# Optimization experiments

Hardware: AMD Instinct MI355X
Metric: run time of the kernel (lower is better)

The kernel has to match this reference:

```python
import jax, jax.numpy as jnp
import numpy as np
from jax import lax

ALPHA = 0.85
C1 = 0.01 ** 2
C2 = 0.03 ** 2


def _avg_pool3(x):
    # F.avg_pool2d(x, 3, 1, 1) with count_include_pad=True: zero-pad, divide by 9.
    s = lax.reduce_window(x, jnp.array(0.0, x.dtype), lax.add,
                          (1, 1, 3, 3), (1, 1, 1, 1),
                          [(0, 0), (0, 0), (1, 1), (1, 1)])
    return s / jnp.array(9.0, x.dtype)


def _ssim(x, y):
    mu_x = _avg_pool3(x)
    mu_y = _avg_pool3(y)
    sigma_x = jnp.clip(_avg_pool3(x * x) - mu_x * mu_x, 0.0, None)
    sigma_y = jnp.clip(_avg_pool3(y * y) - mu_y * mu_y, 0.0, None)
    sigma_xy = _avg_pool3(x * y) - mu_x * mu_y
    ssim_n = (2.0 * mu_x * mu_y + C1) * (2.0 * sigma_xy + C2)
    ssim_d = (mu_x * mu_x + mu_y * mu_y + C1) * (sigma_x + sigma_y + C2)
    return jnp.clip((1.0 - ssim_n / ssim_d) / 2.0, 0.0, 1.0)


def _warp_right(right_img, disp):
    # grid_sample(bilinear, border, align_corners=True) where y maps identically
    # to its own row -> a 1D horizontal bilinear gather at x_sample = x - disp.
    B, C, H, W = right_img.shape
    x_base = jnp.arange(W, dtype=disp.dtype).reshape(1, 1, 1, W)
    x_sample = x_base - disp                      # [B,1,H,W]
    xs = jnp.clip(x_sample, 0.0, W - 1.0)         # border padding
    x0 = jnp.floor(xs)
    w = xs - x0                                   # frac weight
    i0 = x0.astype(jnp.int32)
    i1 = jnp.minimum(i0 + 1, W - 1)
    i0b = jnp.broadcast_to(i0, (B, C, H, W))
    i1b = jnp.broadcast_to(i1, (B, C, H, W))
    g0 = jnp.take_along_axis(right_img, i0b, axis=3)
    g1 = jnp.take_along_axis(right_img, i1b, axis=3)
    warped = (1.0 - w) * g0 + w * g1              # w broadcasts over C
    valid = ((x_sample > 0) & (x_sample < W - 1)).astype(disp.dtype)
    return warped, valid


def setup_inputs() -> dict:
    key = jax.random.key(0)
    k1, k2, k3 = jax.random.split(key, 3)
    B, H, W = 8, 720, 1280
    disp = jax.random.normal(k1, (B, 1, H, W), dtype=jnp.float32)
    left_img = jax.random.uniform(k2, (B, 3, H, W), dtype=jnp.float32)
    right_img = jax.random.uniform(k3, (B, 3, H, W), dtype=jnp.float32)
    return {"disp": disp, "left_img": left_img, "right_img": right_img}


def reference(disp, left_img, right_img):
    right_warped, valid = _warp_right(right_img, disp)
    l1_err = jnp.mean(jnp.abs(left_img - right_warped), axis=1, keepdims=True)
    ssim_err = jnp.mean(_ssim(left_img, right_warped), axis=1, keepdims=True)
    photo_err = ALPHA * ssim_err + (1.0 - ALPHA) * l1_err
    n_valid = jnp.maximum(jnp.sum(valid), 1.0)
    return jnp.sum(photo_err * valid) / n_valid
```

## Files before the change

### kernel.cpp

```cpp
#include <hip/hip_runtime.h>


#define P_ALPHA 0.85f
#define P_C1 1e-4f
#define P_C2 9e-4f

constexpr int W_ = 1280, H_ = 720, HW_ = W_ * H_;
constexpr int UCOLS = 62;
constexpr int RPW   = 12;
constexpr int XS    = 21;
constexpr int YS    = H_ / RPW;
constexpr int TASKS = XS * YS * 8;
constexpr int HALF  = TASKS / 2;
constexpr int NB    = HALF / 4;

__global__ __launch_bounds__(256, 5)
void photo_loss_kernel(const float* __restrict__ disp,
                       const float* __restrict__ left,
                       const float* __restrict__ right,
                       float* __restrict__ acc)
{
    __shared__ float redpv[4], redv[4];

    const int tid  = threadIdx.x;
    const int lane = tid & 63;
    const int wv   = tid >> 6;
    const int wgid = blockIdx.x * 4 + wv;
    const float wm1 = (float)(W_ - 1);

    float sum_pv = 0.f, sum_v = 0.f;

    for (int half = 0; half < 2; ++half) {
        const int t   = wgid + half * HALF;
        const int xs  = t % XS;
        const int rem = t / XS;
        const int ys  = rem % YS;
        const int b   = rem / YS;

        const int base = xs * UCOLS;
        const int col  = base + lane - 1;
        const int r0   = ys * RPW;

        const float* __restrict__ dispb = disp + (size_t)b * HW_;
        const float* __restrict__ L0 = left  + (size_t)(b * 3 + 0) * HW_;
        const float* __restrict__ L1 = left  + (size_t)(b * 3 + 1) * HW_;
        const float* __restrict__ L2 = left  + (size_t)(b * 3 + 2) * HW_;
        const float* __restrict__ R0 = right + (size_t)(b * 3 + 0) * HW_;
        const float* __restrict__ R1 = right + (size_t)(b * 3 + 1) * HW_;
        const float* __restrict__ R2 = right + (size_t)(b * 3 + 2) * HW_;

        const int   colC = min(max(col, 0), W_ - 1);
        const float colv = (col >= 0 && col < W_) ? 1.f : 0.f;
        const float ocm  = (lane >= 1 && lane <= UCOLS && col < W_) ? 1.f : 0.f;

        float rsx[3][3], rsy[3][3], rsxx[3][3], rsyy[3][3], rsxy[3][3];
        float l1r[3], vr[3];

        auto emit = [&](int cs) {
            const float inv9 = 1.f / 9.f;
            float ssim_sum = 0.f;
            #pragma unroll
            for (int c = 0; c < 3; ++c) {
                float mu_x = (rsx[c][0]  + rsx[c][1]  + rsx[c][2])  * inv9;
                float mu_y = (rsy[c][0]  + rsy[c][1]  + rsy[c][2])  * inv9;
                float exx  = (rsxx[c][0] + rsxx[c][1] + rsxx[c][2]) * inv9;
                float eyy  = (rsyy[c][0] + rsyy[c][1] + rsyy[c][2]) * inv9;
                float exy  = (rsxy[c][0] + rsxy[c][1] + rsxy[c][2]) * inv9;
                float sig_x  = fmaxf(exx - mu_x * mu_x, 0.f);
                float sig_y  = fmaxf(eyy - mu_y * mu_y, 0.f);
                float sig_xy = exy - mu_x * mu_y;
                float n  = (2.f * mu_x * mu_y + P_C1) * (2.f * sig_xy + P_C2);
                float dd = (mu_x * mu_x + mu_y * mu_y + P_C1) * (sig_x + sig_y + P_C2);
                float s  = (1.f - n * __builtin_amdgcn_rcpf(dd)) * 0.5f;
                s = fminf(fmaxf(s, 0.f), 1.f);
                ssim_sum += s;
            }
            float photo = P_ALPHA * (ssim_sum * (1.f / 3.f))
                        + (1.f - P_ALPHA) * (l1r[cs] * (1.f / 3.f));
            sum_pv += photo * vr[cs] * ocm;
            sum_v  += vr[cs] * ocm;
        };

        float dC, xC0, xC1, xC2;
        {
            const int rc  = max(r0 - 1, 0);
            const int off = rc * W_ + colC;
            dC = dispb[off]; xC0 = L0[off]; xC1 = L1[off]; xC2 = L2[off];
        }

        #pragma unroll
        for (int j = 0; j <= RPW + 2; ++j) {
            const int s = j % 3;
            const int r = r0 - 1 + j;
            if (j <= RPW + 1) {
                const int   rc = min(max(r, 0), H_ - 1);
                const float rv = (r >= 0 && r < H_) ? 1.f : 0.f;
                const float m  = rv * colv;

                const float xsm = (float)col - dC;
                const float xcl = fminf(fmaxf(xsm, 0.f), wm1);
                const float xf  = floorf(xcl);
                const float fr  = xcl - xf;
                const int   i0  = (int)xf;
                const int   i1  = min(i0 + 1, W_ - 1);
                const int   ro  = rc * W_;
                const float g00 = R0[ro + i0], g01 = R0[ro + i1];
                const float g10 = R1[ro + i0], g11 = R1[ro + i1];
                const float g20 = R2[ro + i0], g21 = R2[ro + i1];

                float dN = 0.f, xN0 = 0.f, xN1 = 0.f, xN2 = 0.f;
                if (j <= RPW) {
                    const int rn   = min(max(r + 1, 0), H_ - 1);
                    const int offn = rn * W_ + colC;
                    dN = dispb[offn];
                    xN0 = L0[offn]; xN1 = L1[offn]; xN2 = L2[offn];
                }

                if (j >= 3) emit((s + 1) % 3);

                const float omf = 1.f - fr;
                const float y0 = (omf * g00 + fr * g01) * m;
                const float y1 = (omf * g10 + fr * g11) * m;
                const float y2 = (omf * g20 + fr * g21) * m;
                const float x0 = xC0 * m;
                const float x1 = xC1 * m;
                const float x2 = xC2 * m;

                float xl, xr, yl, yr;
                xl = __shfl_up(x0, 1, 64); xr = __shfl_down(x0, 1, 64);
                yl = __shfl_up(y0, 1, 64); yr = __shfl_down(y0, 1, 64);
                rsx[0][s]  = xl + x0 + xr;
                rsy[0][s]  = yl + y0 + yr;
                rsxx[0][s] = xl * xl + x0 * x0 + xr * xr;
                rsyy[0][s] = yl * yl + y0 * y0 + yr * yr;
                rsxy[0][s] = xl * yl + x0 * y0 + xr * yr;

                xl = __shfl_up(x1, 1, 64); xr = __shfl_down(x1, 1, 64);
                yl = __shfl_up(y1, 1, 64); yr = __shfl_down(y1, 1, 64);
                rsx[1][s]  = xl + x1 + xr;
                rsy[1][s]  = yl + y1 + yr;
                rsxx[1][s] = xl * xl + x1 * x1 + xr * xr;
                rsyy[1][s] = yl * yl + y1 * y1 + yr * yr;
                rsxy[1][s] = xl * yl + x1 * y1 + xr * yr;

                xl = __shfl_up(x2, 1, 64); xr = __shfl_down(x2, 1, 64);
                yl = __shfl_up(y2, 1, 64); yr = __shfl_down(y2, 1, 64);
                rsx[2][s]  = xl + x2 + xr;
                rsy[2][s]  = yl + y2 + yr;
                rsxx[2][s] = xl * xl + x2 * x2 + xr * xr;
                rsyy[2][s] = yl * yl + y2 * y2 + yr * yr;
                rsxy[2][s] = xl * yl + x2 * y2 + xr * yr;

                l1r[s] = fabsf(x0 - y0) + fabsf(x1 - y1) + fabsf(x2 - y2);
                vr[s]  = (xsm > 0.f && xsm < wm1) ? 1.f : 0.f;

                dC = dN; xC0 = xN0; xC1 = xN1; xC2 = xN2;
            } else {
                emit((s + 1) % 3);
            }
        }
    }

    #pragma unroll
    for (int off = 32; off > 0; off >>= 1) {
        sum_pv += __shfl_down(sum_pv, off, 64);
        sum_v  += __shfl_down(sum_v,  off, 64);
    }
    if (lane == 0) { redpv[wv] = sum_pv; redv[wv] = sum_v; }
    __syncthreads();
    if (tid == 0) {
        atomicAdd(&acc[0], redpv[0] + redpv[1] + redpv[2] + redpv[3]);
        atomicAdd(&acc[1], redv[0]  + redv[1]  + redv[2]  + redv[3]);
    }
}

__global__ void photo_loss_finalize(const float* __restrict__ acc,
                                    float* __restrict__ out)
{
    out[0] = acc[0] / fmaxf(acc[1], 1.f);
}

extern "C" void kernel_launch(void* const* d_in, const int* in_sizes, int n_in,
                              void* d_out, int out_size, void* d_ws, size_t ws_size,
                              hipStream_t stream)
{
    const float* disp  = (const float*)d_in[0];
    const float* left  = (const float*)d_in[1];
    const float* right = (const float*)d_in[2];
    float* out = (float*)d_out;
    float* acc = (float*)d_ws;

    hipMemsetAsync(acc, 0, 2 * sizeof(float), stream);

    dim3 grid(NB);
    dim3 block(256);
    photo_loss_kernel<<<grid, block, 0, stream>>>(disp, left, right, acc);
    photo_loss_finalize<<<1, 1, 0, stream>>>(acc, out);
}
```

Measured before the change: 256.8 us.

## Replace right-image gathers with coalesced row loads and wave shuffles

Each wave now loads a contiguous 64-wide window of the right image per row (coalesced) and performs the bilinear gather via cross-lane shuffles, falling back to global loads only for lanes whose sample index lands outside the window. The output columns per wave are narrowed to leave margin for disparity shifts. The work mapping also changes from two half tasks per wave over a 1D grid to one task per wave on a 3D grid. This targets the cost of scattered global gathers, in exchange for more shuffle instructions, a divergent fallback branch and less useful work per lane.

```diff
diff --git a/kernel.cpp b/kernel.cpp
--- a/kernel.cpp
+++ b/kernel.cpp
@@ -6,15 +6,12 @@
 #define P_C2 9e-4f
 
 constexpr int W_ = 1280, H_ = 720, HW_ = W_ * H_;
-constexpr int UCOLS = 62;
+constexpr int UCOLS = 52;
+constexpr int VLANES = 54;
 constexpr int RPW   = 12;
-constexpr int XS    = 21;
-constexpr int YS    = H_ / RPW;
-constexpr int TASKS = XS * YS * 8;
-constexpr int HALF  = TASKS / 2;
-constexpr int NB    = HALF / 4;
-
-__global__ __launch_bounds__(256, 5)
+constexpr int XS    = 25;
+
+__global__ __launch_bounds__(256)
 void photo_loss_kernel(const float* __restrict__ disp,
                        const float* __restrict__ left,
                        const float* __restrict__ right,
@@ -25,139 +22,153 @@
     const int tid  = threadIdx.x;
     const int lane = tid & 63;
     const int wv   = tid >> 6;
-    const int wgid = blockIdx.x * 4 + wv;
+    const int b    = blockIdx.z;
+    const int obase = blockIdx.x * UCOLS;
+    const int col   = obase - 1 + lane;
+    const int wb    = obase - 6;
+    const int r0    = (blockIdx.y * 4 + wv) * RPW;
     const float wm1 = (float)(W_ - 1);
 
+    const float* __restrict__ dispb = disp + (size_t)b * HW_;
+    const float* __restrict__ L0 = left  + (size_t)(b * 3 + 0) * HW_;
+    const float* __restrict__ L1 = left  + (size_t)(b * 3 + 1) * HW_;
+    const float* __restrict__ L2 = left  + (size_t)(b * 3 + 2) * HW_;
+    const float* __restrict__ R0 = right + (size_t)(b * 3 + 0) * HW_;
+    const float* __restrict__ R1 = right + (size_t)(b * 3 + 1) * HW_;
+    const float* __restrict__ R2 = right + (size_t)(b * 3 + 2) * HW_;
+
+    const int   colC = min(max(col, 0), W_ - 1);
+    const int   wq   = min(max(wb + lane, 0), W_ - 1);
+    const float colv = (col >= 0 && col < W_) ? 1.f : 0.f;
+    const float ocm  = (lane >= 1 && lane <= UCOLS && col < W_) ? 1.f : 0.f;
+    const bool  vlane = (lane < VLANES);
+
+    float rsx[3][3], rsy[3][3], rsxx[3][3], rsyy[3][3], rsxy[3][3];
+    float l1r[3], vr[3];
     float sum_pv = 0.f, sum_v = 0.f;
 
-    for (int half = 0; half < 2; ++half) {
-        const int t   = wgid + half * HALF;
-        const int xs  = t % XS;
-        const int rem = t / XS;
-        const int ys  = rem % YS;
-        const int b   = rem / YS;
-
-        const int base = xs * UCOLS;
-        const int col  = base + lane - 1;
-        const int r0   = ys * RPW;
-
-        const float* __restrict__ dispb = disp + (size_t)b * HW_;
-        const float* __restrict__ L0 = left  + (size_t)(b * 3 + 0) * HW_;
-        const float* __restrict__ L1 = left  + (size_t)(b * 3 + 1) * HW_;
-        const float* __restrict__ L2 = left  + (size_t)(b * 3 + 2) * HW_;
-        const float* __restrict__ R0 = right + (size_t)(b * 3 + 0) * HW_;
-        const float* __restrict__ R1 = right + (size_t)(b * 3 + 1) * HW_;
-        const float* __restrict__ R2 = right + (size_t)(b * 3 + 2) * HW_;
-
-        const int   colC = min(max(col, 0), W_ - 1);
-        const float colv = (col >= 0 && col < W_) ? 1.f : 0.f;
-        const float ocm  = (lane >= 1 && lane <= UCOLS && col < W_) ? 1.f : 0.f;
-
-        float rsx[3][3], rsy[3][3], rsxx[3][3], rsyy[3][3], rsxy[3][3];
-        float l1r[3], vr[3];
-
-        auto emit = [&](int cs) {
-            const float inv9 = 1.f / 9.f;
-            float ssim_sum = 0.f;
-            #pragma unroll
-            for (int c = 0; c < 3; ++c) {
-                float mu_x = (rsx[c][0]  + rsx[c][1]  + rsx[c][2])  * inv9;
-                float mu_y = (rsy[c][0]  + rsy[c][1]  + rsy[c][2])  * inv9;
-                float exx  = (rsxx[c][0] + rsxx[c][1] + rsxx[c][2]) * inv9;
-                float eyy  = (rsyy[c][0] + rsyy[c][1] + rsyy[c][2]) * inv9;
-                float exy  = (rsxy[c][0] + rsxy[c][1] + rsxy[c][2]) * inv9;
-                float sig_x  = fmaxf(exx - mu_x * mu_x, 0.f);
-                float sig_y  = fmaxf(eyy - mu_y * mu_y, 0.f);
-                float sig_xy = exy - mu_x * mu_y;
-                float n  = (2.f * mu_x * mu_y + P_C1) * (2.f * sig_xy + P_C2);
-                float dd = (mu_x * mu_x + mu_y * mu_y + P_C1) * (sig_x + sig_y + P_C2);
-                float s  = (1.f - n * __builtin_amdgcn_rcpf(dd)) * 0.5f;
-                s = fminf(fmaxf(s, 0.f), 1.f);
-                ssim_sum += s;
+    auto emit = [&](int cs) {
+        const float inv9 = 1.f / 9.f;
+        float ssim_sum = 0.f;
+        #pragma unroll
+        for (int c = 0; c < 3; ++c) {
+            float mu_x = (rsx[c][0]  + rsx[c][1]  + rsx[c][2])  * inv9;
+            float mu_y = (rsy[c][0]  + rsy[c][1]  + rsy[c][2])  * inv9;
+            float exx  = (rsxx[c][0] + rsxx[c][1] + rsxx[c][2]) * inv9;
+            float eyy  = (rsyy[c][0] + rsyy[c][1] + rsyy[c][2]) * inv9;
+            float exy  = (rsxy[c][0] + rsxy[c][1] + rsxy[c][2]) * inv9;
+            float sig_x  = fmaxf(exx - mu_x * mu_x, 0.f);
+            float sig_y  = fmaxf(eyy - mu_y * mu_y, 0.f);
+            float sig_xy = exy - mu_x * mu_y;
+            float n  = (2.f * mu_x * mu_y + P_C1) * (2.f * sig_xy + P_C2);
+            float dd = (mu_x * mu_x + mu_y * mu_y + P_C1) * (sig_x + sig_y + P_C2);
+            float s  = (1.f - n * __builtin_amdgcn_rcpf(dd)) * 0.5f;
+            s = fminf(fmaxf(s, 0.f), 1.f);
+            ssim_sum += s;
+        }
+        float photo = P_ALPHA * (ssim_sum * (1.f / 3.f))
+                    + (1.f - P_ALPHA) * (l1r[cs] * (1.f / 3.f));
+        sum_pv += photo * vr[cs] * ocm;
+        sum_v  += vr[cs] * ocm;
+    };
+
+    float dC, xC0, xC1, xC2, rw0, rw1, rw2;
+    {
+        const int rc  = max(r0 - 1, 0);
+        const int off = rc * W_ + colC;
+        dC = dispb[off]; xC0 = L0[off]; xC1 = L1[off]; xC2 = L2[off];
+        const int wo = rc * W_ + wq;
+        rw0 = R0[wo]; rw1 = R1[wo]; rw2 = R2[wo];
+    }
+
+    #pragma unroll
+    for (int j = 0; j <= RPW + 2; ++j) {
+        const int s = j % 3;
+        const int r = r0 - 1 + j;
+        if (j <= RPW + 1) {
+            const int   rc = min(max(r, 0), H_ - 1);
+            const float rv = (r >= 0 && r < H_) ? 1.f : 0.f;
+            const float m  = rv * colv;
+
+            float dN = 0.f, xN0 = 0.f, xN1 = 0.f, xN2 = 0.f;
+            float nw0 = 0.f, nw1 = 0.f, nw2 = 0.f;
+            if (j <= RPW) {
+                const int rn   = min(max(r + 1, 0), H_ - 1);
+                const int offn = rn * W_ + colC;
+                dN = dispb[offn];
+                xN0 = L0[offn]; xN1 = L1[offn]; xN2 = L2[offn];
+                const int won = rn * W_ + wq;
+                nw0 = R0[won]; nw1 = R1[won]; nw2 = R2[won];
             }
-            float photo = P_ALPHA * (ssim_sum * (1.f / 3.f))
-                        + (1.f - P_ALPHA) * (l1r[cs] * (1.f / 3.f));
-            sum_pv += photo * vr[cs] * ocm;
-            sum_v  += vr[cs] * ocm;
-        };
-
-        float dC, xC0, xC1, xC2;
-        {
-            const int rc  = max(r0 - 1, 0);
-            const int off = rc * W_ + colC;
-            dC = dispb[off]; xC0 = L0[off]; xC1 = L1[off]; xC2 = L2[off];
-        }
-
-        #pragma unroll
-        for (int j = 0; j <= RPW + 2; ++j) {
-            const int s = j % 3;
-            const int r = r0 - 1 + j;
-            if (j <= RPW + 1) {
-                const int   rc = min(max(r, 0), H_ - 1);
-                const float rv = (r >= 0 && r < H_) ? 1.f : 0.f;
-                const float m  = rv * colv;
-
-                const float xsm = (float)col - dC;
-                const float xcl = fminf(fmaxf(xsm, 0.f), wm1);
-                const float xf  = floorf(xcl);
-                const float fr  = xcl - xf;
-                const int   i0  = (int)xf;
-                const int   i1  = min(i0 + 1, W_ - 1);
-                const int   ro  = rc * W_;
-                const float g00 = R0[ro + i0], g01 = R0[ro + i1];
-                const float g10 = R1[ro + i0], g11 = R1[ro + i1];
-                const float g20 = R2[ro + i0], g21 = R2[ro + i1];
-
-                float dN = 0.f, xN0 = 0.f, xN1 = 0.f, xN2 = 0.f;
-                if (j <= RPW) {
-                    const int rn   = min(max(r + 1, 0), H_ - 1);
-                    const int offn = rn * W_ + colC;
-                    dN = dispb[offn];
-                    xN0 = L0[offn]; xN1 = L1[offn]; xN2 = L2[offn];
+
+            const float xsm = (float)col - dC;
+            const float xcl = fminf(fmaxf(xsm, 0.f), wm1);
+            const float xf  = floorf(xcl);
+            const float fr  = xcl - xf;
+            const int   i0  = (int)xf;
+            const int   i1  = min(i0 + 1, W_ - 1);
+            const int   sl0 = i0 - wb;
+            const int   sl1 = i1 - wb;
+            const int   sl0c = min(max(sl0, 0), 63);
+            const int   sl1c = min(max(sl1, 0), 63);
+            float g00 = __shfl(rw0, sl0c, 64), g01 = __shfl(rw0, sl1c, 64);
+            float g10 = __shfl(rw1, sl0c, 64), g11 = __shfl(rw1, sl1c, 64);
+            float g20 = __shfl(rw2, sl0c, 64), g21 = __shfl(rw2, sl1c, 64);
+            {
+                const bool outb = vlane && (m > 0.f) &&
+                                  (((unsigned)sl0 > 63u) || ((unsigned)sl1 > 63u));
+                if (__any(outb ? 1 : 0)) {
+                    if (outb) {
+                        const int ro = rc * W_;
+                        g00 = R0[ro + i0]; g01 = R0[ro + i1];
+                        g10 = R1[ro + i0]; g11 = R1[ro + i1];
+                        g20 = R2[ro + i0]; g21 = R2[ro + i1];
+                    }
                 }
-
-                if (j >= 3) emit((s + 1) % 3);
-
-                const float omf = 1.f - fr;
-                const float y0 = (omf * g00 + fr * g01) * m;
-                const float y1 = (omf * g10 + fr * g11) * m;
-                const float y2 = (omf * g20 + fr * g21) * m;
-                const float x0 = xC0 * m;
-                const float x1 = xC1 * m;
-                const float x2 = xC2 * m;
-
-                float xl, xr, yl, yr;
-                xl = __shfl_up(x0, 1, 64); xr = __shfl_down(x0, 1, 64);
-                yl = __shfl_up(y0, 1, 64); yr = __shfl_down(y0, 1, 64);
-                rsx[0][s]  = xl + x0 + xr;
-                rsy[0][s]  = yl + y0 + yr;
-                rsxx[0][s] = xl * xl + x0 * x0 + xr * xr;
-                rsyy[0][s] = yl * yl + y0 * y0 + yr * yr;
-                rsxy[0][s] = xl * yl + x0 * y0 + xr * yr;
-
-                xl = __shfl_up(x1, 1, 64); xr = __shfl_down(x1, 1, 64);
-                yl = __shfl_up(y1, 1, 64); yr = __shfl_down(y1, 1, 64);
-                rsx[1][s]  = xl + x1 + xr;
-                rsy[1][s]  = yl + y1 + yr;
-                rsxx[1][s] = xl * xl + x1 * x1 + xr * xr;
-                rsyy[1][s] = yl * yl + y1 * y1 + yr * yr;
-                rsxy[1][s] = xl * yl + x1 * y1 + xr * yr;
-
-                xl = __shfl_up(x2, 1, 64); xr = __shfl_down(x2, 1, 64);
-                yl = __shfl_up(y2, 1, 64); yr = __shfl_down(y2, 1, 64);
-                rsx[2][s]  = xl + x2 + xr;
-                rsy[2][s]  = yl + y2 + yr;
-                rsxx[2][s] = xl * xl + x2 * x2 + xr * xr;
-                rsyy[2][s] = yl * yl + y2 * y2 + yr * yr;
-                rsxy[2][s] = xl * yl + x2 * y2 + xr * yr;
-
-                l1r[s] = fabsf(x0 - y0) + fabsf(x1 - y1) + fabsf(x2 - y2);
-                vr[s]  = (xsm > 0.f && xsm < wm1) ? 1.f : 0.f;
-
-                dC = dN; xC0 = xN0; xC1 = xN1; xC2 = xN2;
-            } else {
-                emit((s + 1) % 3);
             }
+
+            if (j >= 3) emit((s + 1) % 3);
+
+            const float omf = 1.f - fr;
+            const float y0 = (omf * g00 + fr * g01) * m;
+            const float y1 = (omf * g10 + fr * g11) * m;
+            const float y2 = (omf * g20 + fr * g21) * m;
+            const float x0 = xC0 * m;
+            const float x1 = xC1 * m;
+            const float x2 = xC2 * m;
+
+            float xl, xr, yl, yr;
+            xl = __shfl_up(x0, 1, 64); xr = __shfl_down(x0, 1, 64);
+            yl = __shfl_up(y0, 1, 64); yr = __shfl_down(y0, 1, 64);
+            rsx[0][s]  = xl + x0 + xr;
+            rsy[0][s]  = yl + y0 + yr;
+            rsxx[0][s] = xl * xl + x0 * x0 + xr * xr;
+            rsyy[0][s] = yl * yl + y0 * y0 + yr * yr;
+            rsxy[0][s] = xl * yl + x0 * y0 + xr * yr;
+
+            xl = __shfl_up(x1, 1, 64); xr = __shfl_down(x1, 1, 64);
+            yl = __shfl_up(y1, 1, 64); yr = __shfl_down(y1, 1, 64);
+            rsx[1][s]  = xl + x1 + xr;
+            rsy[1][s]  = yl + y1 + yr;
+            rsxx[1][s] = xl * xl + x1 * x1 + xr * xr;
+            rsyy[1][s] = yl * yl + y1 * y1 + yr * yr;
+            rsxy[1][s] = xl * yl + x1 * y1 + xr * yr;
+
+            xl = __shfl_up(x2, 1, 64); xr = __shfl_down(x2, 1, 64);
+            yl = __shfl_up(y2, 1, 64); yr = __shfl_down(y2, 1, 64);
+            rsx[2][s]  = xl + x2 + xr;
+            rsy[2][s]  = yl + y2 + yr;
+            rsxx[2][s] = xl * xl + x2 * x2 + xr * xr;
+            rsyy[2][s] = yl * yl + y2 * y2 + yr * yr;
+            rsxy[2][s] = xl * yl + x2 * y2 + xr * yr;
+
+            l1r[s] = fabsf(x0 - y0) + fabsf(x1 - y1) + fabsf(x2 - y2);
+            vr[s]  = (xsm > 0.f && xsm < wm1) ? 1.f : 0.f;
+
+            dC = dN; xC0 = xN0; xC1 = xN1; xC2 = xN2;
+            rw0 = nw0; rw1 = nw1; rw2 = nw2;
+        } else {
+            emit((s + 1) % 3);
         }
     }
 
@@ -192,7 +203,7 @@
 
     hipMemsetAsync(acc, 0, 2 * sizeof(float), stream);
 
-    dim3 grid(NB);
+    dim3 grid(XS, H_ / (4 * RPW), 8);
     dim3 block(256);
     photo_loss_kernel<<<grid, block, 0, stream>>>(disp, left, right, acc);
     photo_loss_finalize<<<1, 1, 0, stream>>>(acc, out);
```

Result: slower. 289.5 us (+12.8%).
